# Optimization experiments

Hardware: AMD Instinct MI355X
Metric: run time of the kernel (lower is better)

## Reference

```python
import jax, jax.numpy as jnp
import numpy as np

NUM_HEADS = 32
KV_HEADS = 8
HEAD_DIM = 128
HIDDEN = 4096
Q_DIM = NUM_HEADS * HEAD_DIM      # 4096
KV_DIM = KV_HEADS * HEAD_DIM      # 1024
GROUP = NUM_HEADS // KV_HEADS     # 4 (GQA)
ROPE_THETA = 10000.0
LORA_SCALE = 0.5
BP, S = 4, 1024                   # prefill requests x prefill seq len
BD, L = 64, 2048                  # decode requests x cached kv len
R, NA = 16, 8                     # lora rank, num adapters


def _rope(x, pos):
    # x: [..., n_heads, HEAD_DIM]; pos broadcastable over the token dims of x
    half = x.shape[-1] // 2
    inv = 1.0 / (ROPE_THETA ** (jnp.arange(half, dtype=jnp.float32) / half))
    freqs = pos[..., None].astype(jnp.float32) * inv          # pos.shape + (half,)
    cos = jnp.cos(freqs)[..., None, :]                        # insert head axis
    sin = jnp.sin(freqs)[..., None, :]
    x1, x2 = x[..., :half], x[..., half:]
    return jnp.concatenate([x1 * cos - x2 * sin, x2 * cos + x1 * sin], axis=-1)


def _lora(x, A, B, idx):
    # grouped multi-adapter LoRA: per-request adapter selection
    # x: [b, ..., H]; A: [NA, H, R]; B: [NA, R, D]; idx: [b]
    t = jnp.einsum('b...h,bhr->b...r', x, A[idx])
    return LORA_SCALE * jnp.einsum('b...r,brd->b...d', t, B[idx])


def setup_inputs() -> dict:
    key = jax.random.key(0)
    ks = jax.random.split(key, 16)
    T = BP * S + BD
    w = lambda k, shp: (jax.random.normal(k, shp, jnp.float32) * 0.02)
    return {
        'hidden_states': jax.random.normal(ks[0], (T, HIDDEN), jnp.float32),
        'w_qkv': w(ks[1], (HIDDEN, Q_DIM + 2 * KV_DIM)),
        'w_o': w(ks[2], (Q_DIM, HIDDEN)),
        'k_cache': jax.random.normal(ks[3], (BD, L, KV_HEADS, HEAD_DIM), jnp.float32),
        'v_cache': jax.random.normal(ks[4], (BD, L, KV_HEADS, HEAD_DIM), jnp.float32),
        'lora_a_q': w(ks[5], (NA, HIDDEN, R)),
        'lora_b_q': w(ks[6], (NA, R, Q_DIM)),
        'lora_a_k': w(ks[7], (NA, HIDDEN, R)),
        'lora_b_k': w(ks[8], (NA, R, KV_DIM)),
        'lora_a_v': w(ks[9], (NA, HIDDEN, R)),
        'lora_b_v': w(ks[10], (NA, R, KV_DIM)),
        'lora_a_o': w(ks[11], (NA, Q_DIM, R)),
        'lora_b_o': w(ks[12], (NA, R, HIDDEN)),
        'prefill_adapter_idx': jax.random.randint(ks[13], (BP,), 0, NA),
        'decode_adapter_idx': jax.random.randint(ks[14], (BD,), 0, NA),
    }


def reference(hidden_states, w_qkv, w_o, k_cache, v_cache,
              lora_a_q, lora_b_q, lora_a_k, lora_b_k, lora_a_v, lora_b_v,
              lora_a_o, lora_b_o, prefill_adapter_idx, decode_adapter_idx):
    TP = BP * S
    qkv = hidden_states @ w_qkv
    q, k, v = jnp.split(qkv, [Q_DIM, Q_DIM + KV_DIM], axis=1)

    x_p = hidden_states[:TP].reshape(BP, S, HIDDEN)
    x_d = hidden_states[TP:]

    # apply_lora_weight_kvq: per-request adapters on q/k/v
    q_p = q[:TP].reshape(BP, S, Q_DIM) + _lora(x_p, lora_a_q, lora_b_q, prefill_adapter_idx)
    k_p = k[:TP].reshape(BP, S, KV_DIM) + _lora(x_p, lora_a_k, lora_b_k, prefill_adapter_idx)
    v_p = v[:TP].reshape(BP, S, KV_DIM) + _lora(x_p, lora_a_v, lora_b_v, prefill_adapter_idx)
    q_d = q[TP:] + _lora(x_d, lora_a_q, lora_b_q, decode_adapter_idx)
    k_d = k[TP:] + _lora(x_d, lora_a_k, lora_b_k, decode_adapter_idx)
    v_d = v[TP:] + _lora(x_d, lora_a_v, lora_b_v, decode_adapter_idx)

    scale = 1.0 / np.sqrt(HEAD_DIM).astype(np.float32)

    # ---- prefill: causal self-attention with on-the-fly RoPE ----
    q_p = _rope(q_p.reshape(BP, S, NUM_HEADS, HEAD_DIM), jnp.arange(S, dtype=jnp.float32))
    k_p = _rope(k_p.reshape(BP, S, KV_HEADS, HEAD_DIM), jnp.arange(S, dtype=jnp.float32))
    v_p = v_p.reshape(BP, S, KV_HEADS, HEAD_DIM)
    kr = jnp.repeat(k_p, GROUP, axis=2)
    vr = jnp.repeat(v_p, GROUP, axis=2)
    scores = jnp.einsum('bqhd,bkhd->bhqk', q_p, kr) * scale
    causal = jnp.tril(jnp.ones((S, S), bool))
    scores = jnp.where(causal, scores, -jnp.inf)
    attn = jax.nn.softmax(scores, axis=-1)
    out_p = jnp.einsum('bhqk,bkhd->bqhd', attn, vr).reshape(TP, Q_DIM)

    # ---- decode: one new token per request vs paged KV cache ----
    q_d = _rope(q_d.reshape(BD, NUM_HEADS, HEAD_DIM), jnp.asarray(L, jnp.float32))
    k_new = _rope(k_d.reshape(BD, KV_HEADS, HEAD_DIM), jnp.asarray(L, jnp.float32))
    k_hist = _rope(k_cache, jnp.arange(L, dtype=jnp.float32))
    k_all = jnp.concatenate([k_hist, k_new[:, None]], axis=1)   # [BD, L+1, kvh, hd]
    v_all = jnp.concatenate([v_cache, v_d.reshape(BD, 1, KV_HEADS, HEAD_DIM)], axis=1)
    kr2 = jnp.repeat(k_all, GROUP, axis=2)
    vr2 = jnp.repeat(v_all, GROUP, axis=2)
    s2 = jnp.einsum('bhd,bkhd->bhk', q_d, kr2) * scale
    a2 = jax.nn.softmax(s2, axis=-1)
    out_d = jnp.einsum('bhk,bkhd->bhd', a2, vr2).reshape(BD, Q_DIM)

    # ---- o_proj + apply_lora_weight_attn ----
    attn_raw = jnp.concatenate([out_p, out_d], axis=0)
    o = attn_raw @ w_o
    o_p = o[:TP].reshape(BP, S, HIDDEN) + _lora(attn_raw[:TP].reshape(BP, S, Q_DIM), lora_a_o, lora_b_o, prefill_adapter_idx)
    o_d = o[TP:] + _lora(attn_raw[TP:], lora_a_o, lora_b_o, decode_adapter_idx)
    return jnp.concatenate([o_p.reshape(TP, HIDDEN), o_d], axis=0)
```

## Files before the change

### kernel.cpp

```cpp
#include <hip/hip_runtime.h>

#define NUM_HEADS 32
#define KV_HEADS 8
#define HEAD_DIM 128
#define HIDDEN 4096
#define Q_DIM 4096
#define KV_DIM 1024
#define QKV_DIM 6144
#define GROUP 4
#define BP 4
#define S_LEN 1024
#define BD 64
#define L_CTX 2048
#define RANK 16
#define NA 8
#define TP (BP * S_LEN)
#define T_TOT (TP + BD)
#define M_PAD 4224
#define SCALE 0.08838834764831845f
#define LORA_SCALE 0.5f

typedef float fv4 __attribute__((ext_vector_type(4)));
typedef __bf16 bf16x8 __attribute__((ext_vector_type(8)));
typedef unsigned short usv4 __attribute__((ext_vector_type(4)));
typedef unsigned short u16;

__device__ __forceinline__ float b2f(u16 u) {
    unsigned int x = ((unsigned int)u) << 16;
    return __builtin_bit_cast(float, x);
}
__device__ __forceinline__ u16 f2b(float f) {
    unsigned int u = __builtin_bit_cast(unsigned int, f);
    unsigned int r = u + 0x7fffu + ((u >> 16) & 1u);
    return (u16)(r >> 16);
}
__device__ __forceinline__ void gload_lds16(const void* g, void* l) {
    __builtin_amdgcn_global_load_lds((const __attribute__((address_space(1))) void*)g,
                                     (__attribute__((address_space(3))) void*)l, 16, 0, 0);
}

#define OFF_QKV  ((size_t)0)
#define OFF_ATTN OFF_QKV
#define OFF_HB   ((size_t)51904512)
#define OFF_QP   OFF_HB
#define OFF_WOT  OFF_HB
#define OFF_WQT  ((size_t)86507520)
#define OFF_KP   ((size_t)86507520)
#define OFF_VP   ((size_t)94896128)
#define OFF_QD   ((size_t)103284736)
#define OFF_KD   ((size_t)104333312)
#define OFF_VD   ((size_t)104595456)
#define OFF_T    ((size_t)136839168)
#define OFF_TO   ((size_t)137637888)
#define OFF_COS  ((size_t)137904128)
#define OFF_SIN  ((size_t)138428672)

__global__ void rope_tab_kernel(float* ctab, float* stab) {
    int idx = blockIdx.x * 256 + threadIdx.x;
    if (idx >= 2049 * 64) return;
    int pos = idx >> 6, d = idx & 63;
    float inv = 1.0f / powf(10000.0f, (float)d / 64.0f);
    float f = (float)pos * inv;
    ctab[idx] = cosf(f);
    stab[idx] = sinf(f);
}

__global__ void conv_hidden_kernel(const float* __restrict__ x, u16* __restrict__ y) {
    int gid = blockIdx.x * 256 + threadIdx.x;
    if (gid >= M_PAD * (HIDDEN / 8)) return;
    size_t base = (size_t)gid * 8;
    int row = gid >> 9;
    usv4 lo, hi;
    if (row < T_TOT) {
        fv4 a = *(const fv4*)(x + base);
        fv4 b = *(const fv4*)(x + base + 4);
        lo[0] = f2b(a[0]); lo[1] = f2b(a[1]); lo[2] = f2b(a[2]); lo[3] = f2b(a[3]);
        hi[0] = f2b(b[0]); hi[1] = f2b(b[1]); hi[2] = f2b(b[2]); hi[3] = f2b(b[3]);
    } else {
        lo[0] = 0; lo[1] = 0; lo[2] = 0; lo[3] = 0;
        hi[0] = 0; hi[1] = 0; hi[2] = 0; hi[3] = 0;
    }
    *(usv4*)(y + base) = lo;
    *(usv4*)(y + base + 4) = hi;
}

__global__ __launch_bounds__(256) void transpose_f32_bf16_kernel(const float* __restrict__ in,
                                                                 u16* __restrict__ out,
                                                                 int R, int C) {
    __shared__ float tile[64][65];
    int r0 = blockIdx.y * 64, c0 = blockIdx.x * 64;
    int t = threadIdx.x;
    int tr = t >> 4, tc4 = (t & 15) * 4;
#pragma unroll
    for (int it = 0; it < 4; ++it) {
        int r = tr + it * 16;
        fv4 v = *(const fv4*)(in + (size_t)(r0 + r) * C + c0 + tc4);
        tile[r][tc4 + 0] = v[0]; tile[r][tc4 + 1] = v[1];
        tile[r][tc4 + 2] = v[2]; tile[r][tc4 + 3] = v[3];
    }
    __syncthreads();
#pragma unroll
    for (int it = 0; it < 4; ++it) {
        int c = tr + it * 16;
        usv4 st;
        st[0] = f2b(tile[tc4 + 0][c]); st[1] = f2b(tile[tc4 + 1][c]);
        st[2] = f2b(tile[tc4 + 2][c]); st[3] = f2b(tile[tc4 + 3][c]);
        *(usv4*)(out + (size_t)(c0 + c) * R + r0 + tc4) = st;
    }
}

__global__ void lora_a_kernel(const float* __restrict__ x,
                              const float* __restrict__ Aq, const float* __restrict__ Ak,
                              const float* __restrict__ Av,
                              const int* __restrict__ pidx, const int* __restrict__ didx,
                              float* __restrict__ T) {
    int gid = blockIdx.x * 256 + threadIdx.x;
    const int per_mat = T_TOT * RANK;
    if (gid >= 3 * per_mat) return;
    int mat = gid / per_mat;
    int rem = gid - mat * per_mat;
    int t = rem >> 4, r = rem & 15;
    int a = (t < TP) ? pidx[t >> 10] : didx[t - TP];
    const float* A = (mat == 0) ? Aq : (mat == 1 ? Ak : Av);
    A += (size_t)a * HIDDEN * RANK + r;
    const float* xr = x + (size_t)t * HIDDEN;
    float acc = 0.f;
    for (int h = 0; h < HIDDEN; h += 4) {
        acc += xr[h] * A[(size_t)h * RANK];
        acc += xr[h + 1] * A[(size_t)(h + 1) * RANK];
        acc += xr[h + 2] * A[(size_t)(h + 2) * RANK];
        acc += xr[h + 3] * A[(size_t)(h + 3) * RANK];
    }
    T[(size_t)t * 48 + mat * 16 + r] = acc;
}

template <int OUT_BF16>
__global__ __launch_bounds__(256) void gemm_bt_kernel(const u16* __restrict__ A,
                                                      const u16* __restrict__ BT,
                                                      void* __restrict__ Cp,
                                                      int Mstore, int N, int K) {
    __shared__ __align__(16) u16 As[2][128 * 32];
    __shared__ __align__(16) u16 Bs[2][128 * 32];
    int tid = threadIdx.x;
    int m0 = blockIdx.y * 128, n0 = blockIdx.x * 128;
    int lane = tid & 63, w = tid >> 6, lr = lane & 15, lg = lane >> 4;
    int wr = w >> 1, wc = w & 1;
    int arow = tid >> 2, acol = (tid & 3) * 8;
    const u16* Ab = A + (size_t)(m0 + arow) * K + acol;
    const u16* Bb = BT + (size_t)(n0 + arow) * K + acol;
    fv4 acc[4][4] = {};
    int nt = K / 32;
#define GSTAGE(buf, kk)                                                             \
    {                                                                               \
        char* Ad = (char*)&As[buf][0] + w * 1024;                                   \
        char* Bd = (char*)&Bs[buf][0] + w * 1024;                                   \
        gload_lds16(Ab + (kk), Ad);                                                 \
        gload_lds16(Ab + (size_t)64 * K + (kk), Ad + 4096);                         \
        gload_lds16(Bb + (kk), Bd);                                                 \
        gload_lds16(Bb + (size_t)64 * K + (kk), Bd + 4096);                         \
    }
    GSTAGE(0, 0)
    __syncthreads();
    int cur = 0;
    for (int t = 0; t < nt; ++t) {
        if (t + 1 < nt) GSTAGE(cur ^ 1, (t + 1) * 32)
        bf16x8 af[4], bf[4];
#pragma unroll
        for (int i = 0; i < 4; ++i) {
            af[i] = *(const bf16x8*)&As[cur][(wr * 64 + i * 16 + lr) * 32 + lg * 8];
            bf[i] = *(const bf16x8*)&Bs[cur][(wc * 64 + i * 16 + lr) * 32 + lg * 8];
        }
#pragma unroll
        for (int mi = 0; mi < 4; ++mi)
#pragma unroll
            for (int ni = 0; ni < 4; ++ni)
                acc[mi][ni] = __builtin_amdgcn_mfma_f32_16x16x32_bf16(af[mi], bf[ni], acc[mi][ni], 0, 0, 0);
        __syncthreads();
        cur ^= 1;
    }
#undef GSTAGE
#pragma unroll
    for (int mi = 0; mi < 4; ++mi)
#pragma unroll
        for (int ni = 0; ni < 4; ++ni) {
            int col = n0 + wc * 64 + ni * 16 + lr;
#pragma unroll
            for (int r = 0; r < 4; ++r) {
                int row = m0 + wr * 64 + mi * 16 + lg * 4 + r;
                if (row < Mstore) {
                    if (OUT_BF16)
                        ((u16*)Cp)[(size_t)row * N + col] = f2b(acc[mi][ni][r]);
                    else
                        ((float*)Cp)[(size_t)row * N + col] = acc[mi][ni][r];
                }
            }
        }
}

__global__ __launch_bounds__(256) void lorab_rope_scatter_kernel(
    const u16* __restrict__ qkv, const float* __restrict__ T,
    const float* __restrict__ Bq, const float* __restrict__ Bk, const float* __restrict__ Bv,
    const int* __restrict__ pidx, const int* __restrict__ didx,
    const float* __restrict__ ctab, const float* __restrict__ stab,
    u16* __restrict__ qp, u16* __restrict__ kp, u16* __restrict__ vp,
    float* __restrict__ qd, float* __restrict__ kd, float* __restrict__ vd) {
    int t = blockIdx.x;
    __shared__ float Ts[48];
    if (threadIdx.x < 48) Ts[threadIdx.x] = T[(size_t)t * 48 + threadIdx.x];
    __syncthreads();
    bool pre = t < TP;
    int a = pre ? pidx[t >> 10] : didx[t - TP];
    int pos = pre ? (t & 1023) : L_CTX;
    int b = t >> 10;
    int td = t - TP;
    const u16* qrow = qkv + (size_t)t * QKV_DIM;
    for (int p = threadIdx.x; p < 3072; p += 256) {
        if (p < 2048) {
            int h = p >> 6, d = p & 63;
            int col = h * 128 + d;
            float v1 = b2f(qrow[col]), v2 = b2f(qrow[col + 64]);
            const float* B = Bq + (size_t)a * RANK * Q_DIM;
            float l1 = 0.f, l2 = 0.f;
#pragma unroll
            for (int r = 0; r < 16; ++r) {
                float tv = Ts[r];
                l1 += tv * B[(size_t)r * Q_DIM + col];
                l2 += tv * B[(size_t)r * Q_DIM + col + 64];
            }
            v1 += LORA_SCALE * l1; v2 += LORA_SCALE * l2;
            float c = ctab[pos * 64 + d], s = stab[pos * 64 + d];
            float o1 = v1 * c - v2 * s, o2 = v2 * c + v1 * s;
            if (pre) {
                size_t base = (((size_t)(b * 32 + h)) * 1024 + pos) * 128 + d;
                qp[base] = f2b(o1); qp[base + 64] = f2b(o2);
            } else {
                size_t base = ((size_t)(td * 32 + h)) * 128 + d;
                qd[base] = o1; qd[base + 64] = o2;
            }
        } else if (p < 2560) {
            int pp = p - 2048;
            int h = pp >> 6, d = pp & 63;
            int jc = h * 128 + d;
            int col = Q_DIM + jc;
            float v1 = b2f(qrow[col]), v2 = b2f(qrow[col + 64]);
            const float* B = Bk + (size_t)a * RANK * KV_DIM;
            float l1 = 0.f, l2 = 0.f;
#pragma unroll
            for (int r = 0; r < 16; ++r) {
                float tv = Ts[16 + r];
                l1 += tv * B[(size_t)r * KV_DIM + jc];
                l2 += tv * B[(size_t)r * KV_DIM + jc + 64];
            }
            v1 += LORA_SCALE * l1; v2 += LORA_SCALE * l2;
            float c = ctab[pos * 64 + d], s = stab[pos * 64 + d];
            float o1 = v1 * c - v2 * s, o2 = v2 * c + v1 * s;
            if (pre) {
                size_t base = (((size_t)(b * 8 + h)) * 1024 + pos) * 128 + d;
                kp[base] = f2b(o1); kp[base + 64] = f2b(o2);
            } else {
                size_t base = ((size_t)(td * 8 + h)) * 128 + d;
                kd[base] = o1; kd[base + 64] = o2;
            }
        } else {
            int pp = p - 2560;
            int h = pp >> 6, d = pp & 63;
            int jc = h * 128 + d;
            int col = Q_DIM + KV_DIM + jc;
            float v1 = b2f(qrow[col]), v2 = b2f(qrow[col + 64]);
            const float* B = Bv + (size_t)a * RANK * KV_DIM;
            float l1 = 0.f, l2 = 0.f;
#pragma unroll
            for (int r = 0; r < 16; ++r) {
                float tv = Ts[32 + r];
                l1 += tv * B[(size_t)r * KV_DIM + jc];
                l2 += tv * B[(size_t)r * KV_DIM + jc + 64];
            }
            v1 += LORA_SCALE * l1; v2 += LORA_SCALE * l2;
            if (pre) {
                size_t base = (((size_t)(b * 8 + h)) * 1024 + pos) * 128 + d;
                vp[base] = f2b(v1); vp[base + 64] = f2b(v2);
            } else {
                size_t base = ((size_t)(td * 8 + h)) * 128 + d;
                vd[base] = v1; vd[base + 64] = v2;
            }
        }
    }
}

__global__ __launch_bounds__(256) void prefill_attn_kernel(const u16* __restrict__ qp,
                                                           const u16* __restrict__ kp,
                                                           const u16* __restrict__ vp,
                                                           u16* __restrict__ attn) {
    int qblk = blockIdx.x, h = blockIdx.y, b = blockIdx.z;
    int kvh = h >> 2;
    int tid = threadIdx.x, w = tid >> 6, lane = tid & 63, lr = lane & 15, lg = lane >> 4;
    int q0 = qblk * 64 + w * 16;
    int qc = q0 + lr;
    const u16* Q = qp + ((size_t)(b * 32 + h)) * 1024 * 128;
    const u16* K = kp + ((size_t)(b * 8 + kvh)) * 1024 * 128;
    const u16* V = vp + ((size_t)(b * 8 + kvh)) * 1024 * 128;
    bf16x8 qf[4];
#pragma unroll
    for (int dc = 0; dc < 4; ++dc)
        qf[dc] = *(const bf16x8*)(Q + (size_t)qc * 128 + dc * 32 + lg * 8);
    fv4 o[8] = {};
    float m = -INFINITY, lsum = 0.f;
    int nkb = (q0 + 47) >> 5;
    for (int kb = 0; kb < nkb; ++kb) {
        int k0 = kb * 32;
        fv4 s0 = {}, s1 = {};
#pragma unroll
        for (int dc = 0; dc < 4; ++dc) {
            bf16x8 kf0 = *(const bf16x8*)(K + (size_t)(k0 + lr) * 128 + dc * 32 + lg * 8);
            bf16x8 kf1 = *(const bf16x8*)(K + (size_t)(k0 + 16 + lr) * 128 + dc * 32 + lg * 8);
            s0 = __builtin_amdgcn_mfma_f32_16x16x32_bf16(kf0, qf[dc], s0, 0, 0, 0);
            s1 = __builtin_amdgcn_mfma_f32_16x16x32_bf16(kf1, qf[dc], s1, 0, 0, 0);
        }
        float p0[4], p1[4];
        float lm = -INFINITY;
#pragma unroll
        for (int r = 0; r < 4; ++r) {
            float x = s0[r] * SCALE;
            if (k0 + lg * 4 + r > qc) x = -INFINITY;
            p0[r] = x; lm = fmaxf(lm, x);
            x = s1[r] * SCALE;
            if (k0 + 16 + lg * 4 + r > qc) x = -INFINITY;
            p1[r] = x; lm = fmaxf(lm, x);
        }
        lm = fmaxf(lm, __shfl_xor(lm, 16));
        lm = fmaxf(lm, __shfl_xor(lm, 32));
        float mn = fmaxf(m, lm);
        float sc = __expf(m - mn);
        float rs = 0.f;
#pragma unroll
        for (int r = 0; r < 4; ++r) {
            p0[r] = __expf(p0[r] - mn);
            p1[r] = __expf(p1[r] - mn);
            rs += p0[r] + p1[r];
        }
        rs += __shfl_xor(rs, 16);
        rs += __shfl_xor(rs, 32);
        lsum = lsum * sc + rs;
        m = mn;
#pragma unroll
        for (int c = 0; c < 8; ++c) o[c] *= sc;
        bf16x8 pf;
#pragma unroll
        for (int r = 0; r < 4; ++r) {
            pf[r] = (__bf16)p0[r];
            pf[4 + r] = (__bf16)p1[r];
        }
#pragma unroll
        for (int c = 0; c < 8; ++c) {
            bf16x8 vf;
#pragma unroll
            for (int i = 0; i < 4; ++i) {
                vf[i] = __builtin_bit_cast(__bf16, V[(size_t)(k0 + lg * 4 + i) * 128 + c * 16 + lr]);
                vf[4 + i] = __builtin_bit_cast(__bf16, V[(size_t)(k0 + 16 + lg * 4 + i) * 128 + c * 16 + lr]);
            }
            o[c] = __builtin_amdgcn_mfma_f32_16x16x32_bf16(vf, pf, o[c], 0, 0, 0);
        }
    }
    float inv = 1.0f / lsum;
    size_t trow = (size_t)(b * 1024 + qc) * Q_DIM;
#pragma unroll
    for (int c = 0; c < 8; ++c)
#pragma unroll
        for (int r = 0; r < 4; ++r) {
            int feat = h * 128 + c * 16 + lg * 4 + r;
            attn[trow + feat] = f2b(o[c][r] * inv);
        }
}

__global__ __launch_bounds__(512) void decode_attn_kernel(const float* __restrict__ kc,
                                                          const float* __restrict__ vc,
                                                          const float* __restrict__ qd,
                                                          const float* __restrict__ kd,
                                                          const float* __restrict__ vd,
                                                          const float* __restrict__ ctab,
                                                          const float* __restrict__ stab,
                                                          u16* __restrict__ attn) {
    int blk = blockIdx.x;
    int b = blk >> 3, kvh = blk & 7;
    int tid = threadIdx.x, wv = tid >> 6, lane = tid & 63;
    float q1[4], q2[4];
#pragma unroll
    for (int g = 0; g < 4; ++g) {
        size_t qb = ((size_t)(b * 32 + kvh * 4 + g)) * 128;
        q1[g] = qd[qb + lane];
        q2[g] = qd[qb + 64 + lane];
    }
    float m[4], l[4], o1[4], o2[4];
#pragma unroll
    for (int g = 0; g < 4; ++g) { m[g] = -INFINITY; l[g] = 0.f; o1[g] = 0.f; o2[g] = 0.f; }
    for (int key = wv; key <= L_CTX; key += 8) {
        float kr1, kr2, v1, v2;
        if (key < L_CTX) {
            size_t base = (((size_t)b * L_CTX + key) * 8 + kvh) * 128;
            float k1 = kc[base + lane], k2 = kc[base + 64 + lane];
            float c = ctab[key * 64 + lane], s = stab[key * 64 + lane];
            kr1 = k1 * c - k2 * s;
            kr2 = k2 * c + k1 * s;
            v1 = vc[base + lane];
            v2 = vc[base + 64 + lane];
        } else {
            size_t base = ((size_t)(b * 8 + kvh)) * 128;
            kr1 = kd[base + lane]; kr2 = kd[base + 64 + lane];
            v1 = vd[base + lane]; v2 = vd[base + 64 + lane];
        }
#pragma unroll
        for (int g = 0; g < 4; ++g) {
            float part = q1[g] * kr1 + q2[g] * kr2;
#pragma unroll
            for (int off = 32; off; off >>= 1) part += __shfl_xor(part, off);
            float sg = part * SCALE;
            float mn = fmaxf(m[g], sg);
            float sc = __expf(m[g] - mn);
            float p = __expf(sg - mn);
            l[g] = l[g] * sc + p;
            o1[g] = o1[g] * sc + p * v1;
            o2[g] = o2[g] * sc + p * v2;
            m[g] = mn;
        }
    }
    __shared__ float lm[8][4], ll[8][4];
    __shared__ float lo[8][4][128];
#pragma unroll
    for (int g = 0; g < 4; ++g) {
        lo[wv][g][lane] = o1[g];
        lo[wv][g][64 + lane] = o2[g];
    }
    if (lane == 0)
#pragma unroll
        for (int g = 0; g < 4; ++g) { lm[wv][g] = m[g]; ll[wv][g] = l[g]; }
    __syncthreads();
    int g = tid >> 7, d = tid & 127;
    float M = -INFINITY;
#pragma unroll
    for (int wvi = 0; wvi < 8; ++wvi) M = fmaxf(M, lm[wvi][g]);
    float L = 0.f, O = 0.f;
#pragma unroll
    for (int wvi = 0; wvi < 8; ++wvi) {
        float e = __expf(lm[wvi][g] - M);
        L += ll[wvi][g] * e;
        O += lo[wvi][g][d] * e;
    }
    attn[(size_t)(TP + b) * Q_DIM + (kvh * 4 + g) * 128 + d] = f2b(O / L);
}

__global__ void lora_o_a_kernel(const u16* __restrict__ attn, const float* __restrict__ Ao,
                                const int* __restrict__ pidx, const int* __restrict__ didx,
                                float* __restrict__ To) {
    int gid = blockIdx.x * 256 + threadIdx.x;
    if (gid >= T_TOT * RANK) return;
    int t = gid >> 4, r = gid & 15;
    int a = (t < TP) ? pidx[t >> 10] : didx[t - TP];
    const float* A = Ao + (size_t)a * Q_DIM * RANK + r;
    const u16* xr = attn + (size_t)t * Q_DIM;
    float acc = 0.f;
    for (int j = 0; j < Q_DIM; j += 4) {
        acc += b2f(xr[j]) * A[(size_t)j * RANK];
        acc += b2f(xr[j + 1]) * A[(size_t)(j + 1) * RANK];
        acc += b2f(xr[j + 2]) * A[(size_t)(j + 2) * RANK];
        acc += b2f(xr[j + 3]) * A[(size_t)(j + 3) * RANK];
    }
    To[(size_t)t * RANK + r] = acc;
}

__global__ void final_lora_add_kernel(float* __restrict__ out, const float* __restrict__ To,
                                      const float* __restrict__ Bo,
                                      const int* __restrict__ pidx, const int* __restrict__ didx) {
    int gid = blockIdx.x * 256 + threadIdx.x;
    if (gid >= T_TOT * HIDDEN) return;
    int t = gid >> 12, j = gid & 4095;
    int a = (t < TP) ? pidx[t >> 10] : didx[t - TP];
    const float* B = Bo + (size_t)a * RANK * HIDDEN;
    const float* Tr = To + (size_t)t * RANK;
    float acc = 0.f;
#pragma unroll
    for (int r = 0; r < 16; ++r) acc += Tr[r] * B[(size_t)r * HIDDEN + j];
    out[gid] += LORA_SCALE * acc;
}

extern "C" void kernel_launch(void* const* d_in, const int* in_sizes, int n_in,
                              void* d_out, int out_size, void* d_ws, size_t ws_size,
                              hipStream_t stream) {
    const float* hidden = (const float*)d_in[0];
    const float* w_qkv = (const float*)d_in[1];
    const float* w_o = (const float*)d_in[2];
    const float* k_cache = (const float*)d_in[3];
    const float* v_cache = (const float*)d_in[4];
    const float* Aq = (const float*)d_in[5];
    const float* Bq = (const float*)d_in[6];
    const float* Ak = (const float*)d_in[7];
    const float* Bk = (const float*)d_in[8];
    const float* Av = (const float*)d_in[9];
    const float* Bv = (const float*)d_in[10];
    const float* Ao = (const float*)d_in[11];
    const float* Bo = (const float*)d_in[12];
    const int* pidx = (const int*)d_in[13];
    const int* didx = (const int*)d_in[14];
    float* out = (float*)d_out;

    char* ws = (char*)d_ws;
    u16* qkv = (u16*)(ws + OFF_QKV);
    u16* attn = (u16*)(ws + OFF_ATTN);
    u16* hb = (u16*)(ws + OFF_HB);
    u16* wqT = (u16*)(ws + OFF_WQT);
    u16* woT = (u16*)(ws + OFF_WOT);
    float* T = (float*)(ws + OFF_T);
    u16* qp = (u16*)(ws + OFF_QP);
    u16* kp = (u16*)(ws + OFF_KP);
    u16* vp = (u16*)(ws + OFF_VP);
    float* qd = (float*)(ws + OFF_QD);
    float* kd = (float*)(ws + OFF_KD);
    float* vd = (float*)(ws + OFF_VD);
    float* To = (float*)(ws + OFF_TO);
    float* ctab = (float*)(ws + OFF_COS);
    float* stab = (float*)(ws + OFF_SIN);

    rope_tab_kernel<<<513, 256, 0, stream>>>(ctab, stab);
    conv_hidden_kernel<<<(M_PAD * (HIDDEN / 8) + 255) / 256, 256, 0, stream>>>(hidden, hb);
    transpose_f32_bf16_kernel<<<dim3(QKV_DIM / 64, HIDDEN / 64), 256, 0, stream>>>(w_qkv, wqT, HIDDEN, QKV_DIM);
    lora_a_kernel<<<(3 * T_TOT * RANK + 255) / 256, 256, 0, stream>>>(hidden, Aq, Ak, Av, pidx, didx, T);
    gemm_bt_kernel<1><<<dim3(QKV_DIM / 128, M_PAD / 128), 256, 0, stream>>>(hb, wqT, qkv, M_PAD, QKV_DIM, HIDDEN);
    lorab_rope_scatter_kernel<<<T_TOT, 256, 0, stream>>>(qkv, T, Bq, Bk, Bv, pidx, didx,
                                                         ctab, stab, qp, kp, vp, qd, kd, vd);
    prefill_attn_kernel<<<dim3(16, 32, 4), 256, 0, stream>>>(qp, kp, vp, attn);
    decode_attn_kernel<<<512, 512, 0, stream>>>(k_cache, v_cache, qd, kd, vd, ctab, stab, attn);
    transpose_f32_bf16_kernel<<<dim3(HIDDEN / 64, Q_DIM / 64), 256, 0, stream>>>(w_o, woT, Q_DIM, HIDDEN);
    lora_o_a_kernel<<<(T_TOT * RANK + 255) / 256, 256, 0, stream>>>(attn, Ao, pidx, didx, To);
    gemm_bt_kernel<0><<<dim3(HIDDEN / 128, M_PAD / 128), 256, 0, stream>>>(attn, woT, out, T_TOT, HIDDEN, Q_DIM);
    final_lora_add_kernel<<<(T_TOT * HIDDEN + 255) / 256, 256, 0, stream>>>(out, To, Bo, pidx, didx);
}
```

Baseline: 1.768 ms.

## Restructure LoRA-A reductions and GQA-share prefill attention K/V across heads

The LoRA-A and LoRA-O-A kernels now stage four tokens of activations in shared memory. Each lane reads contiguous 16-wide adapter rows with vector loads, and the partial sums are reduced with wave shuffles, replacing strided scalar per-output dot products. The prefill attention kernel now maps the four query heads of a KV group to the four waves of one block, so they share K/V loads through cache. Each wave processes two 16-row query tiles to reuse K and V fragments, and causal tiles are interleaved heavy/light for load balance. This raises register pressure (two accumulator sets, all V fragments preloaded), which risks lower occupancy.

```diff
diff --git a/kernel.cpp b/kernel.cpp
--- a/kernel.cpp
+++ b/kernel.cpp
@@ -109,29 +109,56 @@
     }
 }
 
-__global__ void lora_a_kernel(const float* __restrict__ x,
+__global__ __launch_bounds__(256) void lora_a_kernel(const float* __restrict__ x,
                               const float* __restrict__ Aq, const float* __restrict__ Ak,
                               const float* __restrict__ Av,
                               const int* __restrict__ pidx, const int* __restrict__ didx,
                               float* __restrict__ T) {
-    int gid = blockIdx.x * 256 + threadIdx.x;
-    const int per_mat = T_TOT * RANK;
-    if (gid >= 3 * per_mat) return;
-    int mat = gid / per_mat;
-    int rem = gid - mat * per_mat;
-    int t = rem >> 4, r = rem & 15;
-    int a = (t < TP) ? pidx[t >> 10] : didx[t - TP];
-    const float* A = (mat == 0) ? Aq : (mat == 1 ? Ak : Av);
-    A += (size_t)a * HIDDEN * RANK + r;
-    const float* xr = x + (size_t)t * HIDDEN;
-    float acc = 0.f;
-    for (int h = 0; h < HIDDEN; h += 4) {
-        acc += xr[h] * A[(size_t)h * RANK];
-        acc += xr[h + 1] * A[(size_t)(h + 1) * RANK];
-        acc += xr[h + 2] * A[(size_t)(h + 2) * RANK];
-        acc += xr[h + 3] * A[(size_t)(h + 3) * RANK];
-    }
-    T[(size_t)t * 48 + mat * 16 + r] = acc;
+    __shared__ float xs[4][HIDDEN];
+    int t0 = blockIdx.x * 4;
+    int tid = threadIdx.x;
+    for (int j = tid; j < 4096; j += 256) {
+        int tok = j >> 10, off = (j & 1023) * 4;
+        *(fv4*)&xs[tok][off] = *(const fv4*)(x + (size_t)(t0 + tok) * HIDDEN + off);
+    }
+    __syncthreads();
+    int w = tid >> 6, lane = tid & 63;
+    if (w >= 3) return;
+    const float* Ab = (w == 0) ? Aq : (w == 1 ? Ak : Av);
+    float acc[4][16];
+#pragma unroll
+    for (int tk = 0; tk < 4; ++tk)
+#pragma unroll
+        for (int r = 0; r < 16; ++r) acc[tk][r] = 0.f;
+#pragma unroll
+    for (int tk = 0; tk < 4; ++tk) {
+        int t = t0 + tk;
+        int a = (t < TP) ? pidx[t >> 10] : didx[t - TP];
+        const float* A = Ab + (size_t)a * HIDDEN * RANK;
+        for (int i = 0; i < 64; ++i) {
+            int hh = i * 64 + lane;
+            float xv = xs[tk][hh];
+            const float* Ar = A + (size_t)hh * RANK;
+            fv4 a0 = *(const fv4*)Ar, a1 = *(const fv4*)(Ar + 4);
+            fv4 a2 = *(const fv4*)(Ar + 8), a3 = *(const fv4*)(Ar + 12);
+#pragma unroll
+            for (int r = 0; r < 4; ++r) {
+                acc[tk][r] += xv * a0[r];
+                acc[tk][4 + r] += xv * a1[r];
+                acc[tk][8 + r] += xv * a2[r];
+                acc[tk][12 + r] += xv * a3[r];
+            }
+        }
+    }
+#pragma unroll
+    for (int tk = 0; tk < 4; ++tk)
+#pragma unroll
+        for (int r = 0; r < 16; ++r) {
+            float v = acc[tk][r];
+            v += __shfl_xor(v, 1); v += __shfl_xor(v, 2); v += __shfl_xor(v, 4);
+            v += __shfl_xor(v, 8); v += __shfl_xor(v, 16); v += __shfl_xor(v, 32);
+            if (lane == r) T[(size_t)(t0 + tk) * 48 + w * 16 + r] = v;
+        }
 }
 
 template <int OUT_BF16>
@@ -291,84 +318,132 @@
                                                            const u16* __restrict__ kp,
                                                            const u16* __restrict__ vp,
                                                            u16* __restrict__ attn) {
-    int qblk = blockIdx.x, h = blockIdx.y, b = blockIdx.z;
-    int kvh = h >> 2;
+    int bx = blockIdx.x;
+    int qt = (bx & 1) ? (31 - (bx >> 1)) : (bx >> 1);
+    int kvh = blockIdx.y, b = blockIdx.z;
     int tid = threadIdx.x, w = tid >> 6, lane = tid & 63, lr = lane & 15, lg = lane >> 4;
-    int q0 = qblk * 64 + w * 16;
-    int qc = q0 + lr;
+    int h = kvh * 4 + w;
     const u16* Q = qp + ((size_t)(b * 32 + h)) * 1024 * 128;
     const u16* K = kp + ((size_t)(b * 8 + kvh)) * 1024 * 128;
     const u16* V = vp + ((size_t)(b * 8 + kvh)) * 1024 * 128;
-    bf16x8 qf[4];
-#pragma unroll
-    for (int dc = 0; dc < 4; ++dc)
-        qf[dc] = *(const bf16x8*)(Q + (size_t)qc * 128 + dc * 32 + lg * 8);
-    fv4 o[8] = {};
-    float m = -INFINITY, lsum = 0.f;
-    int nkb = (q0 + 47) >> 5;
+    int qc0 = qt * 32 + lr, qc1 = qt * 32 + 16 + lr;
+    bf16x8 qf0[4], qf1[4];
+#pragma unroll
+    for (int dc = 0; dc < 4; ++dc) {
+        qf0[dc] = *(const bf16x8*)(Q + (size_t)qc0 * 128 + dc * 32 + lg * 8);
+        qf1[dc] = *(const bf16x8*)(Q + (size_t)qc1 * 128 + dc * 32 + lg * 8);
+    }
+    fv4 o0[8] = {}, o1[8] = {};
+    float m0 = -INFINITY, l0 = 0.f;
+    float m1 = -INFINITY, l1 = 0.f;
+    int nkb = qt + 1;
     for (int kb = 0; kb < nkb; ++kb) {
         int k0 = kb * 32;
-        fv4 s0 = {}, s1 = {};
+        fv4 s00 = {}, s10 = {}, s01 = {}, s11 = {};
 #pragma unroll
         for (int dc = 0; dc < 4; ++dc) {
             bf16x8 kf0 = *(const bf16x8*)(K + (size_t)(k0 + lr) * 128 + dc * 32 + lg * 8);
             bf16x8 kf1 = *(const bf16x8*)(K + (size_t)(k0 + 16 + lr) * 128 + dc * 32 + lg * 8);
-            s0 = __builtin_amdgcn_mfma_f32_16x16x32_bf16(kf0, qf[dc], s0, 0, 0, 0);
-            s1 = __builtin_amdgcn_mfma_f32_16x16x32_bf16(kf1, qf[dc], s1, 0, 0, 0);
-        }
-        float p0[4], p1[4];
-        float lm = -INFINITY;
-#pragma unroll
-        for (int r = 0; r < 4; ++r) {
-            float x = s0[r] * SCALE;
-            if (k0 + lg * 4 + r > qc) x = -INFINITY;
-            p0[r] = x; lm = fmaxf(lm, x);
-            x = s1[r] * SCALE;
-            if (k0 + 16 + lg * 4 + r > qc) x = -INFINITY;
-            p1[r] = x; lm = fmaxf(lm, x);
-        }
-        lm = fmaxf(lm, __shfl_xor(lm, 16));
-        lm = fmaxf(lm, __shfl_xor(lm, 32));
-        float mn = fmaxf(m, lm);
-        float sc = __expf(m - mn);
-        float rs = 0.f;
-#pragma unroll
-        for (int r = 0; r < 4; ++r) {
-            p0[r] = __expf(p0[r] - mn);
-            p1[r] = __expf(p1[r] - mn);
-            rs += p0[r] + p1[r];
-        }
-        rs += __shfl_xor(rs, 16);
-        rs += __shfl_xor(rs, 32);
-        lsum = lsum * sc + rs;
-        m = mn;
-#pragma unroll
-        for (int c = 0; c < 8; ++c) o[c] *= sc;
-        bf16x8 pf;
-#pragma unroll
-        for (int r = 0; r < 4; ++r) {
-            pf[r] = (__bf16)p0[r];
-            pf[4 + r] = (__bf16)p1[r];
+            s00 = __builtin_amdgcn_mfma_f32_16x16x32_bf16(kf0, qf0[dc], s00, 0, 0, 0);
+            s10 = __builtin_amdgcn_mfma_f32_16x16x32_bf16(kf1, qf0[dc], s10, 0, 0, 0);
+            s01 = __builtin_amdgcn_mfma_f32_16x16x32_bf16(kf0, qf1[dc], s01, 0, 0, 0);
+            s11 = __builtin_amdgcn_mfma_f32_16x16x32_bf16(kf1, qf1[dc], s11, 0, 0, 0);
+        }
+        bf16x8 vf[8];
+#pragma unroll
+        for (int c = 0; c < 8; ++c)
+#pragma unroll
+            for (int i = 0; i < 4; ++i) {
+                vf[c][i] = __builtin_bit_cast(__bf16, V[(size_t)(k0 + lg * 4 + i) * 128 + c * 16 + lr]);
+                vf[c][4 + i] = __builtin_bit_cast(__bf16, V[(size_t)(k0 + 16 + lg * 4 + i) * 128 + c * 16 + lr]);
+            }
+        bf16x8 pf0, pf1;
+        {
+            float p0[4], p1[4];
+            float lm = -INFINITY;
+#pragma unroll
+            for (int r = 0; r < 4; ++r) {
+                float x = s00[r] * SCALE;
+                if (k0 + lg * 4 + r > qc0) x = -INFINITY;
+                p0[r] = x; lm = fmaxf(lm, x);
+                x = s10[r] * SCALE;
+                if (k0 + 16 + lg * 4 + r > qc0) x = -INFINITY;
+                p1[r] = x; lm = fmaxf(lm, x);
+            }
+            lm = fmaxf(lm, __shfl_xor(lm, 16));
+            lm = fmaxf(lm, __shfl_xor(lm, 32));
+            float mn = fmaxf(m0, lm);
+            float sc = __expf(m0 - mn);
+            float rs = 0.f;
+#pragma unroll
+            for (int r = 0; r < 4; ++r) {
+                p0[r] = __expf(p0[r] - mn);
+                p1[r] = __expf(p1[r] - mn);
+                rs += p0[r] + p1[r];
+            }
+            rs += __shfl_xor(rs, 16);
+            rs += __shfl_xor(rs, 32);
+            l0 = l0 * sc + rs;
+            m0 = mn;
+#pragma unroll
+            for (int c = 0; c < 8; ++c) o0[c] *= sc;
+#pragma unroll
+            for (int r = 0; r < 4; ++r) {
+                pf0[r] = (__bf16)p0[r];
+                pf0[4 + r] = (__bf16)p1[r];
+            }
+        }
+        {
+            float p0[4], p1[4];
+            float lm = -INFINITY;
+#pragma unroll
+            for (int r = 0; r < 4; ++r) {
+                float x = s01[r] * SCALE;
+                if (k0 + lg * 4 + r > qc1) x = -INFINITY;
+                p0[r] = x; lm = fmaxf(lm, x);
+                x = s11[r] * SCALE;
+                if (k0 + 16 + lg * 4 + r > qc1) x = -INFINITY;
+                p1[r] = x; lm = fmaxf(lm, x);
+            }
+            lm = fmaxf(lm, __shfl_xor(lm, 16));
+            lm = fmaxf(lm, __shfl_xor(lm, 32));
+            float mn = fmaxf(m1, lm);
+            float sc = __expf(m1 - mn);
+            float rs = 0.f;
+#pragma unroll
+            for (int r = 0; r < 4; ++r) {
+                p0[r] = __expf(p0[r] - mn);
+                p1[r] = __expf(p1[r] - mn);
+                rs += p0[r] + p1[r];
+            }
+            rs += __shfl_xor(rs, 16);
+            rs += __shfl_xor(rs, 32);
+            l1 = l1 * sc + rs;
+            m1 = mn;
+#pragma unroll
+            for (int c = 0; c < 8; ++c) o1[c] *= sc;
+#pragma unroll
+            for (int r = 0; r < 4; ++r) {
+                pf1[r] = (__bf16)p0[r];
+                pf1[4 + r] = (__bf16)p1[r];
+            }
         }
 #pragma unroll
         for (int c = 0; c < 8; ++c) {
-            bf16x8 vf;
-#pragma unroll
-            for (int i = 0; i < 4; ++i) {
-                vf[i] = __builtin_bit_cast(__bf16, V[(size_t)(k0 + lg * 4 + i) * 128 + c * 16 + lr]);
-                vf[4 + i] = __builtin_bit_cast(__bf16, V[(size_t)(k0 + 16 + lg * 4 + i) * 128 + c * 16 + lr]);
-            }
-            o[c] = __builtin_amdgcn_mfma_f32_16x16x32_bf16(vf, pf, o[c], 0, 0, 0);
-        }
-    }
-    float inv = 1.0f / lsum;
-    size_t trow = (size_t)(b * 1024 + qc) * Q_DIM;
+            o0[c] = __builtin_amdgcn_mfma_f32_16x16x32_bf16(vf[c], pf0, o0[c], 0, 0, 0);
+            o1[c] = __builtin_amdgcn_mfma_f32_16x16x32_bf16(vf[c], pf1, o1[c], 0, 0, 0);
+        }
+    }
+    float inv0 = 1.0f / l0, inv1 = 1.0f / l1;
+    size_t trow0 = (size_t)(b * 1024 + qc0) * Q_DIM;
+    size_t trow1 = (size_t)(b * 1024 + qc1) * Q_DIM;
 #pragma unroll
     for (int c = 0; c < 8; ++c)
 #pragma unroll
         for (int r = 0; r < 4; ++r) {
             int feat = h * 128 + c * 16 + lg * 4 + r;
-            attn[trow + feat] = f2b(o[c][r] * inv);
+            attn[trow0 + feat] = f2b(o0[c][r] * inv0);
+            attn[trow1 + feat] = f2b(o1[c][r] * inv1);
         }
 }
 
@@ -448,23 +523,54 @@
     attn[(size_t)(TP + b) * Q_DIM + (kvh * 4 + g) * 128 + d] = f2b(O / L);
 }
 
-__global__ void lora_o_a_kernel(const u16* __restrict__ attn, const float* __restrict__ Ao,
+__global__ __launch_bounds__(64) void lora_o_a_kernel(const u16* __restrict__ attn,
+                                const float* __restrict__ Ao,
                                 const int* __restrict__ pidx, const int* __restrict__ didx,
                                 float* __restrict__ To) {
-    int gid = blockIdx.x * 256 + threadIdx.x;
-    if (gid >= T_TOT * RANK) return;
-    int t = gid >> 4, r = gid & 15;
-    int a = (t < TP) ? pidx[t >> 10] : didx[t - TP];
-    const float* A = Ao + (size_t)a * Q_DIM * RANK + r;
-    const u16* xr = attn + (size_t)t * Q_DIM;
-    float acc = 0.f;
-    for (int j = 0; j < Q_DIM; j += 4) {
-        acc += b2f(xr[j]) * A[(size_t)j * RANK];
-        acc += b2f(xr[j + 1]) * A[(size_t)(j + 1) * RANK];
-        acc += b2f(xr[j + 2]) * A[(size_t)(j + 2) * RANK];
-        acc += b2f(xr[j + 3]) * A[(size_t)(j + 3) * RANK];
-    }
-    To[(size_t)t * RANK + r] = acc;
+    __shared__ float xs[4][HIDDEN];
+    int t0 = blockIdx.x * 4;
+    int lane = threadIdx.x;
+    for (int j = lane; j < 4096; j += 64) {
+        int tok = j >> 10, off = (j & 1023) * 4;
+        usv4 v = *(const usv4*)(attn + (size_t)(t0 + tok) * Q_DIM + off);
+        xs[tok][off] = b2f(v[0]); xs[tok][off + 1] = b2f(v[1]);
+        xs[tok][off + 2] = b2f(v[2]); xs[tok][off + 3] = b2f(v[3]);
+    }
+    __syncthreads();
+    float acc[4][16];
+#pragma unroll
+    for (int tk = 0; tk < 4; ++tk)
+#pragma unroll
+        for (int r = 0; r < 16; ++r) acc[tk][r] = 0.f;
+#pragma unroll
+    for (int tk = 0; tk < 4; ++tk) {
+        int t = t0 + tk;
+        int a = (t < TP) ? pidx[t >> 10] : didx[t - TP];
+        const float* A = Ao + (size_t)a * Q_DIM * RANK;
+        for (int i = 0; i < 64; ++i) {
+            int hh = i * 64 + lane;
+            float xv = xs[tk][hh];
+            const float* Ar = A + (size_t)hh * RANK;
+            fv4 a0 = *(const fv4*)Ar, a1 = *(const fv4*)(Ar + 4);
+            fv4 a2 = *(const fv4*)(Ar + 8), a3 = *(const fv4*)(Ar + 12);
+#pragma unroll
+            for (int r = 0; r < 4; ++r) {
+                acc[tk][r] += xv * a0[r];
+                acc[tk][4 + r] += xv * a1[r];
+                acc[tk][8 + r] += xv * a2[r];
+                acc[tk][12 + r] += xv * a3[r];
+            }
+        }
+    }
+#pragma unroll
+    for (int tk = 0; tk < 4; ++tk)
+#pragma unroll
+        for (int r = 0; r < 16; ++r) {
+            float v = acc[tk][r];
+            v += __shfl_xor(v, 1); v += __shfl_xor(v, 2); v += __shfl_xor(v, 4);
+            v += __shfl_xor(v, 8); v += __shfl_xor(v, 16); v += __shfl_xor(v, 32);
+            if (lane == r) To[(size_t)(t0 + tk) * RANK + r] = v;
+        }
 }
 
 __global__ void final_lora_add_kernel(float* __restrict__ out, const float* __restrict__ To,
@@ -522,14 +628,14 @@
     rope_tab_kernel<<<513, 256, 0, stream>>>(ctab, stab);
     conv_hidden_kernel<<<(M_PAD * (HIDDEN / 8) + 255) / 256, 256, 0, stream>>>(hidden, hb);
     transpose_f32_bf16_kernel<<<dim3(QKV_DIM / 64, HIDDEN / 64), 256, 0, stream>>>(w_qkv, wqT, HIDDEN, QKV_DIM);
-    lora_a_kernel<<<(3 * T_TOT * RANK + 255) / 256, 256, 0, stream>>>(hidden, Aq, Ak, Av, pidx, didx, T);
+    lora_a_kernel<<<T_TOT / 4, 256, 0, stream>>>(hidden, Aq, Ak, Av, pidx, didx, T);
     gemm_bt_kernel<1><<<dim3(QKV_DIM / 128, M_PAD / 128), 256, 0, stream>>>(hb, wqT, qkv, M_PAD, QKV_DIM, HIDDEN);
     lorab_rope_scatter_kernel<<<T_TOT, 256, 0, stream>>>(qkv, T, Bq, Bk, Bv, pidx, didx,
                                                          ctab, stab, qp, kp, vp, qd, kd, vd);
-    prefill_attn_kernel<<<dim3(16, 32, 4), 256, 0, stream>>>(qp, kp, vp, attn);
+    prefill_attn_kernel<<<dim3(32, 8, 4), 256, 0, stream>>>(qp, kp, vp, attn);
     decode_attn_kernel<<<512, 512, 0, stream>>>(k_cache, v_cache, qd, kd, vd, ctab, stab, attn);
     transpose_f32_bf16_kernel<<<dim3(HIDDEN / 64, Q_DIM / 64), 256, 0, stream>>>(w_o, woT, Q_DIM, HIDDEN);
-    lora_o_a_kernel<<<(T_TOT * RANK + 255) / 256, 256, 0, stream>>>(attn, Ao, pidx, didx, To);
+    lora_o_a_kernel<<<T_TOT / 4, 64, 0, stream>>>(attn, Ao, pidx, didx, To);
     gemm_bt_kernel<0><<<dim3(HIDDEN / 128, M_PAD / 128), 256, 0, stream>>>(attn, woT, out, T_TOT, HIDDEN, Q_DIM);
     final_lora_add_kernel<<<(T_TOT * HIDDEN + 255) / 256, 256, 0, stream>>>(out, To, Bo, pidx, didx);
 }
```

Measured after the change: 1.664 ms. 1.06x faster.
